# Kernel tuning notes

Hardware: AMD Instinct MI355X
Metric: run time of the kernel (lower is better)

## Reference

```python
import jax, jax.numpy as jnp
import numpy as np

N, E, H, OUT, L = 50000, 500000, 256, 128, 2
EPS = 1e-5  # torch LayerNorm default


def _make_edges(k):
    # both rows cover all N nodes so that unique()/remap in the original is identity
    k1, k2, kp = jax.random.split(k, 3)
    row0 = jnp.concatenate([jax.random.permutation(kp, N), jax.random.randint(k1, (E - N,), 0, N)])
    row1 = jnp.concatenate([jnp.arange(N), jax.random.randint(k2, (E - N,), 0, N)])
    return jnp.stack([row0, row1]).astype(jnp.int32)


def setup_inputs() -> dict:
    key = jax.random.key(0)
    ks = jax.random.split(key, 7)
    s = 0.02
    x = jax.random.normal(ks[0], (N, H), jnp.float32)
    edge_r1 = _make_edges(ks[1])
    edge_r2 = _make_edges(ks[2])
    Wl = jax.random.normal(ks[3], (L, H, H), jnp.float32) * s
    W0 = jax.random.normal(ks[4], (L, H, H), jnp.float32) * s
    W1 = jax.random.normal(ks[5], (L, H, H), jnp.float32) * s
    bl = jnp.zeros((L, H), jnp.float32)
    b0 = jnp.zeros((L, H), jnp.float32)
    b1 = jnp.zeros((L, H), jnp.float32)
    gamma = jnp.ones((L, H), jnp.float32)
    beta = jnp.zeros((L, H), jnp.float32)
    Wout = jax.random.normal(ks[6], (OUT, H), jnp.float32) * s
    bout = jnp.zeros((OUT,), jnp.float32)
    return dict(x=x, edge_r1=edge_r1, edge_r2=edge_r2, Wl=Wl, bl=bl, W0=W0, b0=b0,
                W1=W1, b1=b1, gamma=gamma, beta=beta, Wout=Wout, bout=bout)


def _layer(i, h, x0, e, Wl, bl, W0, b0, W1, b1, gamma, beta):
    # PyG flow='target_to_source', aggr='add': gather h at e[1], scatter-add at e[0]
    agg = jax.ops.segment_sum(h[e[1]], e[0], num_segments=h.shape[0])  # [N, H]
    z = agg @ Wl[i].T + bl[i] + h @ W0[i].T + b0[i] + x0 @ W1[i].T + b1[i]
    z = jax.nn.relu(z)
    mu = jnp.mean(z, axis=-1, keepdims=True)
    var = jnp.mean(jnp.square(z - mu), axis=-1, keepdims=True)
    return (z - mu) * jax.lax.rsqrt(var + EPS) * gamma[i] + beta[i]  # dropout is identity in eval


def reference(x, edge_r1, edge_r2, Wl, bl, W0, b0, W1, b1, gamma, beta, Wout, bout):
    # reversed(metapath): (C,r2,C) with conv_idx=1 first, then (C,r1,C) with conv_idx=0
    h = _layer(1, x, x, edge_r2, Wl, bl, W0, b0, W1, b1, gamma, beta)
    h = _layer(0, h, x, edge_r1, Wl, bl, W0, b0, W1, b1, gamma, beta)
    return h @ Wout.T + bout  # [N, OUT]
```

## Files before the change

### kernel.cpp

```cpp
#include <hip/hip_runtime.h>
#include <stdint.h>

#define N_NODES 50000
#define N_EDGES 500000
#define NPAD    50048
#define NBLK    128
#define EPB     4096
#define NBUCK   391
#define LFLAT   50048
#define NSC2    196
#define P4CAP   4096
#define EPS     1e-5f

typedef _Float16 half8_ __attribute__((ext_vector_type(8)));
typedef _Float16 half4_ __attribute__((ext_vector_type(4)));
typedef float    float4_ __attribute__((ext_vector_type(4)));

typedef uint32_t u32_g __attribute__((address_space(1)));
typedef uint32_t u32_s __attribute__((address_space(3)));

__device__ __forceinline__ void gload16(const void* g, void* lds_wave_base) {
    __builtin_amdgcn_global_load_lds((const u32_g*)g, (u32_s*)lds_wave_base, 16, 0, 0);
}

__global__ __launch_bounds__(256) void prep_kernel(
        const int* __restrict__ e1, const int* __restrict__ e2,
        int* __restrict__ G, unsigned short* __restrict__ rank16,
        const float* __restrict__ x, _Float16* __restrict__ xh,
        _Float16* __restrict__ aggb, _Float16* __restrict__ h1,
        const float* __restrict__ Wl, const float* __restrict__ W0,
        const float* __restrict__ W1, const float* __restrict__ Wout,
        _Float16* __restrict__ Wcat,
        const float* __restrict__ bl, const float* __restrict__ b0,
        const float* __restrict__ b1, const float* __restrict__ bout,
        float* __restrict__ bias) {
    __shared__ int hist[NBUCK];
    const int bid = blockIdx.x;
    const int tid = threadIdx.x;
    if (bid < 256) {
        const int s = bid >> 7, blk = bid & 127;
        const int* dst = s ? e2 : e1;
        unsigned short* rk = rank16 + (size_t)s * N_EDGES;
        for (int b = tid; b < NBUCK; b += 256) hist[b] = 0;
        __syncthreads();
        const int e0 = blk * EPB;
        int myrank[16];
#pragma unroll
        for (int k = 0; k < 16; k++) {
            int i = e0 + k * 256 + tid;
            int r = 0;
            if (i < N_EDGES) r = atomicAdd(&hist[dst[i] >> 7], 1);
            myrank[k] = r;
        }
#pragma unroll
        for (int k = 0; k < 16; k++) {
            int i = e0 + k * 256 + tid;
            if (i < N_EDGES) rk[i] = (unsigned short)myrank[k];
        }
        __syncthreads();
        int* Gp = G + (s * NBLK + blk) * NBUCK;
        for (int b = tid; b < NBUCK; b += 256) Gp[b] = hist[b];
    } else if (bid < 12756) {
        int i = (bid - 256) * 256 + tid;
        float4_ v = ((const float4_*)x)[i];
        half4_ h;
        h[0] = (_Float16)v[0]; h[1] = (_Float16)v[1];
        h[2] = (_Float16)v[2]; h[3] = (_Float16)v[3];
        ((half4_*)xh)[i] = h;
    } else if (bid < 14420) {
        int i = (bid - 12756) * 256 + tid;
        if (i < 2 * 256 * 768) {
            int l = i / (256 * 768);
            int r = i % (256 * 768);
            int j = r / 768, k = r % 768;
            const float* s = (k < 256) ? Wl : (k < 512 ? W0 : W1);
            Wcat[i] = (_Float16)s[l * 65536 + j * 256 + (k & 255)];
        } else {
            Wcat[i] = (_Float16)Wout[i - 2 * 256 * 768];
        }
    } else if (bid < 14456) {
        int j = (bid - 14420) * 256 + tid;
        int buf = j / 3072, jj = j % 3072;
        _Float16* p = (buf == 0) ? xh : (buf == 1) ? aggb : h1;
        half4_ z = {(_Float16)0.f, (_Float16)0.f, (_Float16)0.f, (_Float16)0.f};
        *(half4_*)(p + (size_t)N_NODES * 256 + (size_t)jj * 4) = z;
    } else {
        int i = (bid - 14456) * 256 + tid;
        if (i < 512)      bias[i] = bl[i] + b0[i] + b1[i];
        else if (i < 640) bias[i] = bout[i - 512];
    }
}

__global__ __launch_bounds__(256) void p2_scan(const int* __restrict__ G,
                                               unsigned long long* __restrict__ state,
                                               int* __restrict__ start2) {
    __shared__ int sm[256];
    __shared__ int s_excl;
    const int bid = blockIdx.x;
    const int s = bid / NSC2;
    const int seq = bid % NSC2;
    const int t = threadIdx.x;
    const int i = seq * 256 + t;
    unsigned long long* st = state + s * NSC2;

    int v = 0;
    if (i < LFLAT) v = G[(s * NBLK + (i & 127)) * NBUCK + (i >> 7)];
    sm[t] = v;
    __syncthreads();
    for (int off = 1; off < 256; off <<= 1) {
        int x = sm[t];
        if (t >= off) x += sm[t - off];
        __syncthreads();
        sm[t] = x;
        __syncthreads();
    }
    int total = sm[255];

    if (t == 0) {
        if (seq == 0) {
            atomicExch(&st[0], (2ULL << 32) | (unsigned int)total);
            s_excl = 0;
        } else {
            atomicExch(&st[seq], (1ULL << 32) | (unsigned int)total);
            int running = 0;
            int j = seq - 1;
            while (true) {
                unsigned long long sv = atomicAdd(&st[j], 0ULL);
                unsigned int tag = (unsigned int)(sv >> 32);
                if (tag == 0) continue;
                running += (int)(unsigned int)sv;
                if (tag == 2) break;
                j--;
            }
            atomicExch(&st[seq], (2ULL << 32) | (unsigned int)(running + total));
            s_excl = running;
        }
    }
    __syncthreads();
    if (i < LFLAT) start2[s * LFLAT + i] = s_excl + sm[t] - v;
}

__global__ __launch_bounds__(256) void p3_scatter(const int* __restrict__ e1,
                                                  const int* __restrict__ e2,
                                                  const unsigned short* __restrict__ rank16,
                                                  const int* __restrict__ start2,
                                                  unsigned int* __restrict__ tmp) {
    const int bid = blockIdx.x;
    const int s = bid >> 7, blk = bid & 127;
    const int t = threadIdx.x;
    const int* ed = s ? e2 : e1;
    const int* st = start2 + s * LFLAT;
    const unsigned short* rk = rank16 + (size_t)s * N_EDGES;
    unsigned int* tp = tmp + (size_t)s * N_EDGES;
    const int e0 = blk * EPB;
#pragma unroll
    for (int k = 0; k < 16; k++) {
        int i = e0 + k * 256 + t;
        if (i < N_EDGES) {
            int d   = ed[i];
            int src = ed[N_EDGES + i];
            int pos = st[(d >> 7) * NBLK + blk] + (int)rk[i];
            tp[pos] = ((unsigned)(d & 127) << 16) | (unsigned)src;
        }
    }
}

__global__ __launch_bounds__(256) void p4_build(const unsigned int* __restrict__ tmp,
                                                const int* __restrict__ start2,
                                                int* __restrict__ rp,
                                                int* __restrict__ col) {
    __shared__ int cnt[128];
    __shared__ int off[128];
    __shared__ unsigned int   stM[P4CAP];
    __shared__ unsigned short stS[P4CAP];
    const int b = blockIdx.x;
    const int s = blockIdx.y;
    const int t = threadIdx.x;
    const int* st = start2 + s * LFLAT;
    const int A   = st[b * NBLK];
    const int Bnd = (b == NBUCK - 1) ? N_EDGES : st[(b + 1) * NBLK];
    const unsigned int* tp = tmp + (size_t)s * N_EDGES;

    if (t < 128) cnt[t] = 0;
    __syncthreads();
    for (int eb = A; eb < Bnd; eb += 256) {
        int e = eb + t;
        if (e < Bnd) {
            unsigned v = tp[e];
            int idx = (int)(v >> 16);
            int r = atomicAdd(&cnt[idx], 1);
            int sl = e - A;
            if (sl < P4CAP) {
                stM[sl] = ((unsigned)idx << 12) | (unsigned)r;
                stS[sl] = (unsigned short)(v & 0xFFFFu);
            }
        }
    }
    __syncthreads();
    if (t < 128) off[t] = cnt[t];
    __syncthreads();
    for (int d = 1; d < 128; d <<= 1) {
        int x = 0;
        if (t < 128) { x = off[t]; if (t >= d) x += off[t - d]; }
        __syncthreads();
        if (t < 128) off[t] = x;
        __syncthreads();
    }
    const int nE = Bnd - A;
    int* colS = col + (size_t)s * N_EDGES;
    for (int sl = t; sl < nE && sl < P4CAP; sl += 256) {
        unsigned m = stM[sl];
        int idx = (int)(m >> 12), r = (int)(m & 4095u);
        colS[A + off[idx] - cnt[idx] + r] = (int)stS[sl];
    }
    const int nbase = b * 128;
    if (t < 128 && nbase + t < N_NODES)
        rp[s * (N_NODES + 1) + nbase + t] = A + off[t] - cnt[t];
    if (b == NBUCK - 1 && t == 0) rp[s * (N_NODES + 1) + N_NODES] = N_EDGES;
}

__global__ void gather_kernel(const _Float16* __restrict__ hin,
                              const int* __restrict__ rowptr, const int* __restrict__ col,
                              _Float16* __restrict__ dst, int n) {
    int node = blockIdx.x * 4 + (threadIdx.x >> 6);
    int lane = threadIdx.x & 63;
    int half = lane >> 5, l5 = lane & 31;
    if (node >= n) return;
    int s = rowptr[node], e = rowptr[node + 1];
    float a[8] = {0.f, 0.f, 0.f, 0.f, 0.f, 0.f, 0.f, 0.f};
    float b[8] = {0.f, 0.f, 0.f, 0.f, 0.f, 0.f, 0.f, 0.f};
    int i = s + half;
    for (; i + 6 < e; i += 8) {
        int c0 = col[i], c1 = col[i + 2], c2 = col[i + 4], c3 = col[i + 6];
        half8_ v0 = *(const half8_*)(hin + (size_t)c0 * 256 + l5 * 8);
        half8_ v1 = *(const half8_*)(hin + (size_t)c1 * 256 + l5 * 8);
        half8_ v2 = *(const half8_*)(hin + (size_t)c2 * 256 + l5 * 8);
        half8_ v3 = *(const half8_*)(hin + (size_t)c3 * 256 + l5 * 8);
#pragma unroll
        for (int j = 0; j < 8; j++) {
            a[j] += (float)v0[j] + (float)v2[j];
            b[j] += (float)v1[j] + (float)v3[j];
        }
    }
    for (; i < e; i += 2) {
        int c0 = col[i];
        half8_ v0 = *(const half8_*)(hin + (size_t)c0 * 256 + l5 * 8);
#pragma unroll
        for (int j = 0; j < 8; j++) a[j] += (float)v0[j];
    }
    half8_ o;
#pragma unroll
    for (int j = 0; j < 8; j++) {
        float t = a[j] + b[j];
        t += __shfl_xor(t, 32, 64);
        o[j] = (_Float16)t;
    }
    if (half == 0)
        *(half8_*)(dst + (size_t)node * 256 + l5 * 8) = o;
}

__global__ __launch_bounds__(512) void gemm_ln(const _Float16* __restrict__ agg,
                                               const _Float16* __restrict__ hsrc,
                                               const _Float16* __restrict__ xh,
                                               const _Float16* __restrict__ Bw,
                                               const float* __restrict__ bias,
                                               const float* __restrict__ gamma,
                                               const float* __restrict__ beta,
                                               _Float16* __restrict__ H,
                                               const _Float16* __restrict__ Wfin,
                                               const float* __restrict__ bfin,
                                               float* __restrict__ outp) {
    __shared__ __align__(16) char smem[49152];
    char* AsB = smem;
    char* BsB = smem + 16384;
    const int rowBase = blockIdx.x * 128;
    const int tid  = threadIdx.x;
    const int lane = tid & 63;
    const int w    = tid >> 6;
    const int wm = w & 1, wn = w >> 1;
    const int quad = lane >> 4, mr = lane & 15;
    const int x7 = mr & 7;
    const bool fin = (Wfin != nullptr);

    float4_ acc[4][4];
#pragma unroll
    for (int i = 0; i < 4; i++)
#pragma unroll
        for (int j = 0; j < 4; j++) { float4_ z4 = {0.f, 0.f, 0.f, 0.f}; acc[i][j] = z4; }

    int cA0 = w * 64 + lane, cA1 = cA0 + 512;
    int rA0 = cA0 >> 3, rA1 = cA1 >> 3;
    size_t offA0 = (size_t)(rowBase + rA0) * 256 + (((cA0 & 7) ^ (rA0 & 7)) * 8);
    size_t offA1 = (size_t)(rowBase + rA1) * 256 + (((cA1 & 7) ^ (rA1 & 7)) * 8);
    size_t offB[4];
#pragma unroll
    for (int j = 0; j < 4; j++) {
        int c = j * 512 + w * 64 + lane;
        int r = c >> 3;
        offB[j] = (size_t)r * 768 + (((c & 7) ^ (r & 7)) * 8);
    }
    void* lA0 = AsB + w * 1024;
    void* lA1 = AsB + 8192 + w * 1024;

    for (int k0 = 0; k0 < 768; k0 += 64) {
        const _Float16* src = (k0 < 256) ? agg : (k0 < 512) ? hsrc : xh;
        const int kloc = k0 & 255;
        gload16(src + offA0 + kloc, lA0);
        gload16(src + offA1 + kloc, lA1);
        gload16(Bw + offB[0] + k0, BsB + w * 1024);
        gload16(Bw + offB[1] + k0, BsB + 8192 + w * 1024);
        gload16(Bw + offB[2] + k0, BsB + 16384 + w * 1024);
        gload16(Bw + offB[3] + k0, BsB + 24576 + w * 1024);
        __syncthreads();
#pragma unroll
        for (int s = 0; s < 2; s++) {
            half8_ a[4], b[4];
#pragma unroll
            for (int im = 0; im < 4; im++) {
                int row = wm * 64 + im * 16 + mr;
                a[im] = *(const half8_*)(AsB + row * 128 + (((s * 4 + quad) ^ x7) * 16));
            }
#pragma unroll
            for (int in = 0; in < 4; in++) {
                int row = wn * 64 + in * 16 + mr;
                b[in] = *(const half8_*)(BsB + row * 128 + (((s * 4 + quad) ^ x7) * 16));
            }
#pragma unroll
            for (int im = 0; im < 4; im++)
#pragma unroll
                for (int in = 0; in < 4; in++)
                    acc[im][in] = __builtin_amdgcn_mfma_f32_16x16x32_f16(a[im], b[in], acc[im][in], 0, 0, 0);
        }
        __syncthreads();
    }

    float bv[4], gv[4], bev[4];
#pragma unroll
    for (int in = 0; in < 4; in++) {
        int colg = wn * 64 + in * 16 + mr;
        bv[in]  = bias[colg];
        gv[in]  = gamma[colg];
        bev[in] = beta[colg];
    }
    float* lnbuf   = (float*)AsB;
    float* lnstats = (float*)(AsB + 4096);

#pragma unroll
    for (int im = 0; im < 4; im++)
#pragma unroll
        for (int r = 0; r < 4; r++) {
            float s = 0.f, sq = 0.f;
#pragma unroll
            for (int in = 0; in < 4; in++) {
                float v = acc[im][in][r] + bv[in];
                v = v > 0.f ? v : 0.f;
                s += v; sq += v * v;
            }
            s  += __shfl_xor(s, 1, 64);  sq += __shfl_xor(sq, 1, 64);
            s  += __shfl_xor(s, 2, 64);  sq += __shfl_xor(sq, 2, 64);
            s  += __shfl_xor(s, 4, 64);  sq += __shfl_xor(sq, 4, 64);
            s  += __shfl_xor(s, 8, 64);  sq += __shfl_xor(sq, 8, 64);
            if (mr == 0) {
                int rl = wm * 64 + im * 16 + quad * 4 + r;
                lnbuf[(wn * 128 + rl) * 2]     = s;
                lnbuf[(wn * 128 + rl) * 2 + 1] = sq;
            }
        }
    __syncthreads();
    if (tid < 128) {
        float s  = lnbuf[tid * 2]             + lnbuf[(128 + tid) * 2]
                 + lnbuf[(256 + tid) * 2]     + lnbuf[(384 + tid) * 2];
        float sq = lnbuf[tid * 2 + 1]         + lnbuf[(128 + tid) * 2 + 1]
                 + lnbuf[(256 + tid) * 2 + 1] + lnbuf[(384 + tid) * 2 + 1];
        float mu  = s * (1.0f / 256.0f);
        float var = sq * (1.0f / 256.0f) - mu * mu;
        lnstats[tid * 2]     = mu;
        lnstats[tid * 2 + 1] = rsqrtf(var + EPS);
    }
    __syncthreads();

    _Float16* BsH = (_Float16*)BsB;
#pragma unroll
    for (int p = 0; p < 2; p++) {
        if (wm == p) {
#pragma unroll
            for (int im = 0; im < 4; im++)
#pragma unroll
                for (int r = 0; r < 4; r++) {
                    int rl = im * 16 + quad * 4 + r;
                    float mu = lnstats[(p * 64 + rl) * 2];
                    float rs = lnstats[(p * 64 + rl) * 2 + 1];
#pragma unroll
                    for (int in = 0; in < 4; in++) {
                        float v = acc[im][in][r] + bv[in];
                        v = v > 0.f ? v : 0.f;
                        int cc = wn * 64 + in * 16 + mr;
                        int addr = fin ? (cc ^ ((rl & 7) << 3)) : cc;
                        BsH[rl * 256 + addr] =
                            (_Float16)((v - mu) * rs * gv[in] + bev[in]);
                    }
                }
        }
        __syncthreads();
        if (!fin) {
#pragma unroll
            for (int i = 0; i < 4; i++) {
                int c = i * 512 + tid;
                int row = c >> 5, ch = c & 31;
                half8_ v = *(const half8_*)(BsB + c * 16);
                *(half8_*)(H + (size_t)(rowBase + p * 64 + row) * 256 + ch * 8) = v;
            }
            __syncthreads();
        } else {
            float4_ oacc[4];
#pragma unroll
            for (int j = 0; j < 4; j++) { float4_ z4 = {0.f, 0.f, 0.f, 0.f}; oacc[j] = z4; }
            const int rt = w & 3;
            const int cb = (w >> 2) * 4;
            const int arow = rt * 16 + mr;
            const int sw = (arow & 7) << 3;
#pragma unroll
            for (int k0 = 0; k0 < 256; k0 += 32) {
                half8_ av = *(const half8_*)(BsH + arow * 256 + ((k0 + quad * 8) ^ sw));
#pragma unroll
                for (int j = 0; j < 4; j++) {
                    half8_ bv8 = *(const half8_*)(Wfin + (size_t)((cb + j) * 16 + mr) * 256 + k0 + quad * 8);
                    oacc[j] = __builtin_amdgcn_mfma_f32_16x16x32_f16(av, bv8, oacc[j], 0, 0, 0);
                }
            }
#pragma unroll
            for (int j = 0; j < 4; j++) {
                int colg = (cb + j) * 16 + mr;
                float bb = bfin[colg];
#pragma unroll
                for (int r = 0; r < 4; r++) {
                    int row = rowBase + p * 64 + rt * 16 + quad * 4 + r;
                    if (row < N_NODES) outp[(size_t)row * 128 + colg] = oacc[j][r] + bb;
                }
            }
            __syncthreads();
        }
    }
}

extern "C" void kernel_launch(void* const* d_in, const int* in_sizes, int n_in,
                              void* d_out, int out_size, void* d_ws, size_t ws_size,
                              hipStream_t stream) {
    const float* x    = (const float*)d_in[0];
    const int*   e1   = (const int*)d_in[1];
    const int*   e2   = (const int*)d_in[2];
    const float* Wl   = (const float*)d_in[3];
    const float* bl   = (const float*)d_in[4];
    const float* W0   = (const float*)d_in[5];
    const float* b0   = (const float*)d_in[6];
    const float* W1   = (const float*)d_in[7];
    const float* b1   = (const float*)d_in[8];
    const float* gamma= (const float*)d_in[9];
    const float* beta = (const float*)d_in[10];
    const float* Wout = (const float*)d_in[11];
    const float* bout = (const float*)d_in[12];

    char* ws = (char*)d_ws;
    size_t off = 0;
    auto alloc = [&](size_t bytes) -> char* {
        char* p = ws + off;
        off = (off + bytes + 255) & ~(size_t)255;
        return p;
    };
    _Float16* xh   = (_Float16*)alloc((size_t)NPAD * 256 * 2);
    _Float16* aggb = (_Float16*)alloc((size_t)NPAD * 256 * 2);
    _Float16* h1   = (_Float16*)alloc((size_t)NPAD * 256 * 2);
    _Float16* Wcat = (_Float16*)alloc((size_t)(2 * 256 * 768 + 128 * 256) * 2);
    float*    bias = (float*)alloc(640 * 4);
    unsigned long long* states = (unsigned long long*)alloc((size_t)2 * NSC2 * 8);
    int* G      = (int*)alloc((size_t)2 * NBLK * NBUCK * 4);
    int* start2 = (int*)alloc((size_t)2 * LFLAT * 4);
    int* rp     = (int*)alloc((size_t)2 * (N_NODES + 1) * 4);
    unsigned short* rank16 = (unsigned short*)alloc((size_t)2 * N_EDGES * 2);
    unsigned int*   tmp    = (unsigned int*)alloc((size_t)2 * N_EDGES * 4);
    int* col    = (int*)alloc((size_t)2 * N_EDGES * 4);

    int* rp1 = rp, *rp2 = rp + (N_NODES + 1);
    int* col1 = col, *col2 = col + N_EDGES;

    hipMemsetAsync(states, 0, (size_t)2 * NSC2 * 8, stream);

    prep_kernel<<<14459, 256, 0, stream>>>(e1, e2, G, rank16, x, xh, aggb, h1,
                                           Wl, W0, W1, Wout, Wcat,
                                           bl, b0, b1, bout, bias);
    p2_scan<<<2 * NSC2, 256, 0, stream>>>(G, states, start2);
    p3_scatter<<<256, 256, 0, stream>>>(e1, e2, rank16, start2, tmp);
    p4_build<<<dim3(NBUCK, 2), 256, 0, stream>>>(tmp, start2, rp, col);

    const int nb4 = (N_NODES + 3) / 4;
    const _Float16* WoutH = Wcat + 393216;

    gather_kernel<<<nb4, 256, 0, stream>>>(xh, rp2, col2, aggb, N_NODES);
    gemm_ln<<<391, 512, 0, stream>>>(aggb, xh, xh, Wcat + 196608,
                                     bias + 256, gamma + 256, beta + 256, h1,
                                     nullptr, nullptr, nullptr);
    gather_kernel<<<nb4, 256, 0, stream>>>(h1, rp1, col1, aggb, N_NODES);
    gemm_ln<<<391, 512, 0, stream>>>(aggb, h1, xh, Wcat,
                                     bias, gamma, beta, nullptr,
                                     WoutH, bias + 512, (float*)d_out);
}
```

Baseline: 381.8 us.

## Restructure final output projection to run once per 128-row tile via global staging

The final layer's LayerNorm output is now written to a new global buffer h2 for both 64-row halves, and the output projection runs once per 128-row tile afterwards. Each wave loads its rows back through global_load_lds into LDS and computes a 4x2 MFMA tile, reusing each Wout fragment across four row tiles instead of one per half. This cuts redundant Wout loads and per-half sync overhead, at the cost of an extra global write and read of the activation tile. Separately, the hipMemsetAsync of the scan state is folded into an extra block of the prep kernel to save a launch.

```diff
diff --git a/kernel.cpp b/kernel.cpp
--- a/kernel.cpp
+++ b/kernel.cpp
@@ -33,7 +33,8 @@
         _Float16* __restrict__ Wcat,
         const float* __restrict__ bl, const float* __restrict__ b0,
         const float* __restrict__ b1, const float* __restrict__ bout,
-        float* __restrict__ bias) {
+        float* __restrict__ bias,
+        unsigned long long* __restrict__ states) {
     __shared__ int hist[NBUCK];
     const int bid = blockIdx.x;
     const int tid = threadIdx.x;
@@ -84,10 +85,12 @@
         _Float16* p = (buf == 0) ? xh : (buf == 1) ? aggb : h1;
         half4_ z = {(_Float16)0.f, (_Float16)0.f, (_Float16)0.f, (_Float16)0.f};
         *(half4_*)(p + (size_t)N_NODES * 256 + (size_t)jj * 4) = z;
-    } else {
+    } else if (bid < 14459) {
         int i = (bid - 14456) * 256 + tid;
         if (i < 512)      bias[i] = bl[i] + b0[i] + b1[i];
         else if (i < 640) bias[i] = bout[i - 512];
+    } else {
+        for (int i = tid; i < 2 * NSC2; i += 256) states[i] = 0ULL;
     }
 }
 
@@ -280,7 +283,6 @@
     const int wm = w & 1, wn = w >> 1;
     const int quad = lane >> 4, mr = lane & 15;
     const int x7 = mr & 7;
-    const bool fin = (Wfin != nullptr);
 
     float4_ acc[4][4];
 #pragma unroll
@@ -394,51 +396,62 @@
                     for (int in = 0; in < 4; in++) {
                         float v = acc[im][in][r] + bv[in];
                         v = v > 0.f ? v : 0.f;
-                        int cc = wn * 64 + in * 16 + mr;
-                        int addr = fin ? (cc ^ ((rl & 7) << 3)) : cc;
-                        BsH[rl * 256 + addr] =
+                        BsH[rl * 256 + wn * 64 + in * 16 + mr] =
                             (_Float16)((v - mu) * rs * gv[in] + bev[in]);
                     }
                 }
         }
         __syncthreads();
-        if (!fin) {
-#pragma unroll
-            for (int i = 0; i < 4; i++) {
-                int c = i * 512 + tid;
-                int row = c >> 5, ch = c & 31;
-                half8_ v = *(const half8_*)(BsB + c * 16);
-                *(half8_*)(H + (size_t)(rowBase + p * 64 + row) * 256 + ch * 8) = v;
-            }
+#pragma unroll
+        for (int i = 0; i < 4; i++) {
+            int c = i * 512 + tid;
+            int row = c >> 5, ch = c & 31;
+            half8_ v = *(const half8_*)(BsB + c * 16);
+            *(half8_*)(H + (size_t)(rowBase + p * 64 + row) * 256 + ch * 8) = v;
+        }
+        __syncthreads();
+    }
+
+    if (Wfin != nullptr) {
+        const int wm2 = w & 1;
+        const int wn2 = w >> 1;
+        float4_ oacc[4][2];
+#pragma unroll
+        for (int ir = 0; ir < 4; ir++)
+#pragma unroll
+            for (int ic = 0; ic < 2; ic++) { float4_ z4 = {0.f, 0.f, 0.f, 0.f}; oacc[ir][ic] = z4; }
+        const _Float16* hG = H + (size_t)(rowBase + w * 16 + (lane >> 2)) * 256 + (lane & 3) * 8;
+        void* lA = AsB + w * 1024;
+#pragma unroll
+        for (int k0 = 0; k0 < 256; k0 += 32) {
+            gload16(hG + k0, lA);
             __syncthreads();
-        } else {
-            float4_ oacc[4];
-#pragma unroll
-            for (int j = 0; j < 4; j++) { float4_ z4 = {0.f, 0.f, 0.f, 0.f}; oacc[j] = z4; }
-            const int rt = w & 3;
-            const int cb = (w >> 2) * 4;
-            const int arow = rt * 16 + mr;
-            const int sw = (arow & 7) << 3;
-#pragma unroll
-            for (int k0 = 0; k0 < 256; k0 += 32) {
-                half8_ av = *(const half8_*)(BsH + arow * 256 + ((k0 + quad * 8) ^ sw));
-#pragma unroll
-                for (int j = 0; j < 4; j++) {
-                    half8_ bv8 = *(const half8_*)(Wfin + (size_t)((cb + j) * 16 + mr) * 256 + k0 + quad * 8);
-                    oacc[j] = __builtin_amdgcn_mfma_f32_16x16x32_f16(av, bv8, oacc[j], 0, 0, 0);
+            half8_ a2[4], b2[2];
+#pragma unroll
+            for (int ir = 0; ir < 4; ir++)
+                a2[ir] = *(const half8_*)(AsB + (wm2 * 64 + ir * 16 + mr) * 64 + quad * 16);
+#pragma unroll
+            for (int ic = 0; ic < 2; ic++)
+                b2[ic] = *(const half8_*)(Wfin + (size_t)(wn2 * 32 + ic * 16 + mr) * 256 + k0 + quad * 8);
+#pragma unroll
+            for (int ir = 0; ir < 4; ir++)
+#pragma unroll
+                for (int ic = 0; ic < 2; ic++)
+                    oacc[ir][ic] = __builtin_amdgcn_mfma_f32_16x16x32_f16(a2[ir], b2[ic], oacc[ir][ic], 0, 0, 0);
+            __syncthreads();
+        }
+#pragma unroll
+        for (int ic = 0; ic < 2; ic++) {
+            int colg = wn2 * 32 + ic * 16 + mr;
+            float bb = bfin[colg];
+#pragma unroll
+            for (int ir = 0; ir < 4; ir++) {
+#pragma unroll
+                for (int r = 0; r < 4; r++) {
+                    int row = rowBase + wm2 * 64 + ir * 16 + quad * 4 + r;
+                    if (row < N_NODES) outp[(size_t)row * 128 + colg] = oacc[ir][ic][r] + bb;
                 }
             }
-#pragma unroll
-            for (int j = 0; j < 4; j++) {
-                int colg = (cb + j) * 16 + mr;
-                float bb = bfin[colg];
-#pragma unroll
-                for (int r = 0; r < 4; r++) {
-                    int row = rowBase + p * 64 + rt * 16 + quad * 4 + r;
-                    if (row < N_NODES) outp[(size_t)row * 128 + colg] = oacc[j][r] + bb;
-                }
-            }
-            __syncthreads();
         }
     }
 }
@@ -470,6 +483,7 @@
     _Float16* xh   = (_Float16*)alloc((size_t)NPAD * 256 * 2);
     _Float16* aggb = (_Float16*)alloc((size_t)NPAD * 256 * 2);
     _Float16* h1   = (_Float16*)alloc((size_t)NPAD * 256 * 2);
+    _Float16* h2   = (_Float16*)alloc((size_t)NPAD * 256 * 2);
     _Float16* Wcat = (_Float16*)alloc((size_t)(2 * 256 * 768 + 128 * 256) * 2);
     float*    bias = (float*)alloc(640 * 4);
     unsigned long long* states = (unsigned long long*)alloc((size_t)2 * NSC2 * 8);
@@ -483,11 +497,9 @@
     int* rp1 = rp, *rp2 = rp + (N_NODES + 1);
     int* col1 = col, *col2 = col + N_EDGES;
 
-    hipMemsetAsync(states, 0, (size_t)2 * NSC2 * 8, stream);
-
-    prep_kernel<<<14459, 256, 0, stream>>>(e1, e2, G, rank16, x, xh, aggb, h1,
+    prep_kernel<<<14460, 256, 0, stream>>>(e1, e2, G, rank16, x, xh, aggb, h1,
                                            Wl, W0, W1, Wout, Wcat,
-                                           bl, b0, b1, bout, bias);
+                                           bl, b0, b1, bout, bias, states);
     p2_scan<<<2 * NSC2, 256, 0, stream>>>(G, states, start2);
     p3_scatter<<<256, 256, 0, stream>>>(e1, e2, rank16, start2, tmp);
     p4_build<<<dim3(NBUCK, 2), 256, 0, stream>>>(tmp, start2, rp, col);
@@ -501,6 +513,6 @@
                                      nullptr, nullptr, nullptr);
     gather_kernel<<<nb4, 256, 0, stream>>>(h1, rp1, col1, aggb, N_NODES);
     gemm_ln<<<391, 512, 0, stream>>>(aggb, h1, xh, Wcat,
-                                     bias, gamma, beta, nullptr,
+                                     bias, gamma, beta, h2,
                                      WoutH, bias + 512, (float*)d_out);
 }
```

Result: faster. 319.1 us (median of 2 runs) (-16.4%).
